# Kernel optimization log

Hardware: AMD Instinct MI355X
Metric: run time of the kernel (lower is better)

Reference implementation:

```python
import jax, jax.numpy as jnp
import numpy as np

MAX_DIST = 32  # unidirectional T5-style bucketing: num_buckets = 33
N_HEAD, D_K, D_V = 8, 64, 64


def setup_inputs() -> dict:
    key = jax.random.key(0)
    ks = jax.random.split(key, 9)
    B, S, D = 4, 2048, 512
    q = jax.random.normal(ks[0], (B, S, D), dtype=jnp.float32)
    k = jax.random.normal(ks[1], (B, S, D), dtype=jnp.float32)
    v = jax.random.normal(ks[2], (B, S, D), dtype=jnp.float32)
    mask = jax.random.randint(ks[3], (B, 1, 1, S), 0, 2, dtype=jnp.int32)
    sc = 1.0 / np.sqrt(D)
    Wq = jax.random.normal(ks[4], (D, D), dtype=jnp.float32) * sc
    Wk = jax.random.normal(ks[5], (D, D), dtype=jnp.float32) * sc
    Wv = jax.random.normal(ks[6], (D, D), dtype=jnp.float32) * sc
    Wfc = jax.random.normal(ks[7], (D, D), dtype=jnp.float32) * sc
    rel_bias = jax.random.normal(ks[8], (MAX_DIST + 1, N_HEAD), dtype=jnp.float32)
    return {"q": q, "k": k, "v": v, "mask": mask, "Wq": Wq, "Wk": Wk,
            "Wv": Wv, "Wfc": Wfc, "rel_bias": rel_bias}


def _rel_pos_bias(rel_bias, seq_len):
    # unidirectional: bucket = clamp(max(context - memory, 0), 0, MAX_DIST)
    pos = jnp.arange(seq_len)
    n = pos[:, None] - pos[None, :]              # context - memory = -relative_position
    bucket = jnp.clip(jnp.maximum(n, 0), 0, MAX_DIST)
    vals = rel_bias[bucket]                      # (S, S, H)
    return jnp.transpose(vals, (2, 0, 1))[None]  # (1, H, S, S)


def reference(q, k, v, mask, Wq, Wk, Wv, Wfc, rel_bias):
    B, Sq, _ = q.shape
    Sk = k.shape[1]
    scale = D_K ** (-0.5)
    qh = (q @ Wq).reshape(B, Sq, N_HEAD, D_K).transpose(0, 2, 1, 3)  # bhsd
    kh = (k @ Wk).reshape(B, Sk, N_HEAD, D_K).transpose(0, 2, 1, 3)
    vh = (v @ Wv).reshape(B, Sk, N_HEAD, D_V).transpose(0, 2, 1, 3)
    attn = jnp.einsum('bhqd,bhkd->bhqk', qh, kh) * scale
    attn = attn + _rel_pos_bias(rel_bias, Sq)
    attn = jnp.where(mask == 0, jnp.float32(-1e9), attn)
    attn = jax.nn.softmax(attn, axis=-1)          # dropout is identity at eval
    out = jnp.einsum('bhqk,bhkd->bhqd', attn, vh)
    out = out.transpose(0, 2, 1, 3).reshape(B, Sq, N_HEAD * D_V)
    out = out @ Wfc
    return out, attn
```

## Files before the change

kernel.cpp:

```cpp
#include <hip/hip_runtime.h>
#include <hip/hip_bf16.h>


typedef __attribute__((ext_vector_type(8))) short bfrag;
typedef __attribute__((ext_vector_type(4))) float f32x4;
typedef unsigned int u32;

#define MFMA16(a,b,c) __builtin_amdgcn_mfma_f32_16x16x32_bf16(a,b,c,0,0,0)

#define BAR() do{ asm volatile("s_waitcnt lgkmcnt(0)" ::: "memory"); \
                  __builtin_amdgcn_s_barrier(); }while(0)

__device__ __forceinline__ void gl_lds16(const void* g, void* l){
  __builtin_amdgcn_global_load_lds((const __attribute__((address_space(1))) u32*)g,
                                   (__attribute__((address_space(3))) u32*)l, 16, 0, 0);
}
__device__ __forceinline__ short f2bs(float f){
  u32 u = __float_as_uint(f);
  u = (u + 0x7fffu + ((u>>16)&1u)) >> 16;
  return (short)u;
}
__device__ __forceinline__ float b2f(short s){
  return __uint_as_float(((u32)(unsigned short)s) << 16);
}
__device__ __forceinline__ u32 pack2(float a, float b){
  float2 t; t.x = a; t.y = b;
  __hip_bfloat162 h = __float22bfloat162_rn(t);
  return *(u32*)&h;
}

#define BB 4
#define HH 8
#define SS 2048
#define DD 512

#define WQT_OFF  0u
#define WKT_OFF  524288u
#define WVT_OFF  1048576u
#define WFCT_OFF 1572864u
#define QB_OFF   2097152u
#define KB_OFF   10485760u
#define VB_OFF   18874368u
#define QH_OFF   27262976u
#define KH_OFF   35651584u
#define VT_OFF   44040192u
#define OH_OFF   52428800u

__global__ __launch_bounds__(256) void conv_w_k(const float* w0,const float* w1,
                                                const float* w2,const float* w3, char* ws){
  const float* w; short* o;
  switch(blockIdx.z){
    case 0:  w=w0; o=(short*)(ws+WQT_OFF); break;
    case 1:  w=w1; o=(short*)(ws+WKT_OFF); break;
    case 2:  w=w2; o=(short*)(ws+WVT_OFF); break;
    default: w=w3; o=(short*)(ws+WFCT_OFF); break;
  }
  int t  = blockIdx.x*256 + threadIdx.x;
  int n  = t >> 6;
  int k0 = (t & 63) << 3;
  bfrag v;
  #pragma unroll
  for (int j=0;j<8;++j) v[j] = f2bs(w[(k0+j)*512 + n]);
  *(bfrag*)(o + n*512 + k0) = v;
}

__global__ __launch_bounds__(256) void conv_x_k(const float* x0,const float* x1,
                                                const float* x2, char* ws){
  const float* x; short* o;
  switch(blockIdx.z){
    case 0:  x=x0; o=(short*)(ws+QB_OFF); break;
    case 1:  x=x1; o=(short*)(ws+KB_OFF); break;
    default: x=x2; o=(short*)(ws+VB_OFF); break;
  }
  int i = (blockIdx.x*256 + threadIdx.x) << 3;
  float4 a = *(const float4*)(x+i);
  float4 b = *(const float4*)(x+i+4);
  bfrag v;
  v[0]=f2bs(a.x); v[1]=f2bs(a.y); v[2]=f2bs(a.z); v[3]=f2bs(a.w);
  v[4]=f2bs(b.x); v[5]=f2bs(b.y); v[6]=f2bs(b.z); v[7]=f2bs(b.w);
  *(bfrag*)(o+i) = v;
}

__device__ void gemm_core(const short* A, const short* Bt, char* Cout, int mode, int bid){
  __shared__ __align__(16) char lds[32768];
  int i0, j0;
  if (mode==1){ i0 = (bid&3)<<7; j0 = (bid>>2)<<7; }
  else        { i0 = (bid>>2)<<7; j0 = (bid&3)<<7; }
  int tid = threadIdx.x;
  int l = tid & 63, w = tid >> 6;
  int wr = (w>>1)<<6, wc = (w&1)<<6;
  int l15 = l & 15, l4 = l >> 4;
  f32x4 acc[4][4];
  #pragma unroll
  for(int a=0;a<4;++a)
    #pragma unroll
    for(int b=0;b<4;++b) acc[a][b] = (f32x4){0.f,0.f,0.f,0.f};
  const char* Ab = (const char*)A;
  const char* Bb = (const char*)Bt;
  for (int kk=0; kk<8; ++kk){
    #pragma unroll
    for (int it=0; it<4; ++it){
      int ci = it*256 + tid;
      int row = ci>>3, cc = ci&7;
      gl_lds16(Ab + (size_t)(i0+row)*1024 + kk*128 + ((cc^(row&7))<<4),
               lds + ((it*256 + w*64)<<4));
      gl_lds16(Bb + (size_t)(j0+row)*1024 + kk*128 + ((cc^(row&7))<<4),
               lds + 16384 + ((it*256 + w*64)<<4));
    }
    asm volatile("s_waitcnt vmcnt(0)" ::: "memory");
    __syncthreads();
    #pragma unroll
    for (int kb=0; kb<2; ++kb){
      bfrag af[4], bf[4];
      #pragma unroll
      for (int mi=0;mi<4;++mi){
        int row = wr + mi*16 + l15;
        af[mi] = *(const bfrag*)(lds + row*128 + (((kb*4 + l4) ^ (row&7))<<4));
      }
      #pragma unroll
      for (int ni=0;ni<4;++ni){
        int row = wc + ni*16 + l15;
        bf[ni] = *(const bfrag*)(lds + 16384 + row*128 + (((kb*4 + l4) ^ (row&7))<<4));
      }
      #pragma unroll
      for (int mi=0;mi<4;++mi)
        #pragma unroll
        for (int ni=0;ni<4;++ni)
          acc[mi][ni] = MFMA16(af[mi], bf[ni], acc[mi][ni]);
    }
    __syncthreads();
  }
  #pragma unroll
  for (int mi=0;mi<4;++mi){
    #pragma unroll
    for (int ni=0;ni<4;++ni){
      #pragma unroll
      for (int r=0;r<4;++r){
        int i = i0 + wr + mi*16 + (l4<<2) + r;
        int j = j0 + wc + ni*16 + l15;
        float v = acc[mi][ni][r];
        if (mode==2){
          ((float*)Cout)[(size_t)i*512 + j] = v;
        } else if (mode==0){
          size_t o = ((size_t)(((i>>11)<<3) + (j>>6))*2048 + (size_t)(i&2047))*64 + (j&63);
          ((short*)Cout)[o] = f2bs(v);
        } else {
          size_t o = ((size_t)(((j>>11)<<3) + (i>>6))*64 + (size_t)(i&63))*2048 + (j&2047);
          ((short*)Cout)[o] = f2bs(v);
        }
      }
    }
  }
}

__global__ __launch_bounds__(256,2) void gemm_proj_k(char* ws){
  switch(blockIdx.z){
    case 0:  gemm_core((const short*)(ws+QB_OFF),  (const short*)(ws+WQT_OFF), ws+QH_OFF, 0, blockIdx.x); break;
    case 1:  gemm_core((const short*)(ws+KB_OFF),  (const short*)(ws+WKT_OFF), ws+KH_OFF, 0, blockIdx.x); break;
    default: gemm_core((const short*)(ws+WVT_OFF), (const short*)(ws+VB_OFF),  ws+VT_OFF, 1, blockIdx.x); break;
  }
}
__global__ __launch_bounds__(256,2) void gemm_final_k(char* ws, float* out){
  gemm_core((const short*)(ws+OH_OFF), (const short*)(ws+WFCT_OFF), (char*)out, 2, blockIdx.x);
}

#define MSK_OFF_L   65536
#define BIAS_OFF_L  73728
#define WSUM_OFF_L  73872
#define RECIP_OFF_L 74384
#define LDS_TOTAL   74496

__global__ __launch_bounds__(512,4) void attn_k(char* ws, const int* mask,
                                                const float* rel_bias, float* attn_out){
  extern __shared__ __align__(16) char sm[];
  int tid = threadIdx.x;
  int l = tid & 63, w = tid >> 6;
  int l15 = l & 15, l4 = l >> 4;
  int bh = blockIdx.x, qblk = blockIdx.y;
  int b = bh >> 3, h = bh & 7;
  const short* qhb = (const short*)(ws+QH_OFF) + (size_t)bh*SS*64;
  const char*  khb = ws + KH_OFF + (size_t)bh*SS*128;
  const char*  vtb = ws + VT_OFF + (size_t)bh*64*SS*2;

  {
    const int4* m4 = (const int4*)(mask + b*SS);
    int4 ma = m4[tid];
    float4* mf = (float4*)(sm + MSK_OFF_L);
    mf[tid] = make_float4(ma.x?1.f:0.f, ma.y?1.f:0.f, ma.z?1.f:0.f, ma.w?1.f:0.f);
  }
  if (tid < 33) ((float*)(sm+BIAS_OFF_L))[tid] = rel_bias[tid*HH + h];
  float bias0  = rel_bias[h];
  float bias32 = rel_bias[32*HH + h];
  const float* biasl = (const float*)(sm+BIAS_OFF_L);
  const float* maskl = (const float*)(sm+MSK_OFF_L);

  int qrow = (qblk<<4) + l15;
  bfrag qA0 = *(const bfrag*)(qhb + (size_t)qrow*64 + l4*8);
  bfrag qA1 = *(const bfrag*)(qhb + (size_t)qrow*64 + 32 + l4*8);
  int r0 = qblk<<4;
  int wbase = w << 8;

  __syncthreads();

  float rs = 0.f;
  #pragma unroll 2
  for (int t=0; t<16; ++t){
    int c0 = wbase + (t<<4);
    const char* kr = khb + (size_t)(c0 + l15)*128 + (l4<<4);
    bfrag b0 = *(const bfrag*)(kr);
    bfrag b1 = *(const bfrag*)(kr + 64);
    f32x4 acc = (f32x4){0.f,0.f,0.f,0.f};
    acc = MFMA16(b0, qA0, acc);
    acc = MFMA16(b1, qA1, acc);
    float4 m4v = *(const float4*)(maskl + c0 + (l4<<2));
    float pr[4];
    if (c0 >= r0+16){
      #pragma unroll
      for (int r=0;r<4;++r) pr[r] = __expf(acc[r]*0.125f + bias0);
    } else if (c0 <= r0-47){
      #pragma unroll
      for (int r=0;r<4;++r) pr[r] = __expf(acc[r]*0.125f + bias32);
    } else {
      #pragma unroll
      for (int r=0;r<4;++r){
        int n = (r0 + l15) - (c0 + (l4<<2) + r);
        n = n<0 ? 0 : (n>32 ? 32 : n);
        pr[r] = __expf(acc[r]*0.125f + biasl[n]);
      }
    }
    float p0 = m4v.x*pr[0], p1 = m4v.y*pr[1], p2 = m4v.z*pr[2], p3 = m4v.w*pr[3];
    rs += (p0+p1)+(p2+p3);
    int byte = (c0 + (l4<<2)) << 1;
    int ch = (byte>>4) ^ l15;
    uint2 pk; pk.x = pack2(p0,p1); pk.y = pack2(p2,p3);
    *(uint2*)(sm + l15*4096 + (ch<<4) + (byte&15)) = pk;
  }

  {
    rs += __shfl_xor(rs, 16);
    rs += __shfl_xor(rs, 32);
    float* wsum = (float*)(sm+WSUM_OFF_L);
    if (l < 16) wsum[(w<<4) + l15] = rs;
  }
  BAR();
  if (tid < 16){
    float* wsum = (float*)(sm+WSUM_OFF_L);
    float t2 = 0.f;
    #pragma unroll
    for (int i=0;i<8;++i) t2 += wsum[(i<<4) + tid];
    ((float*)(sm+RECIP_OFF_L))[tid] = 1.f/t2;
  }
  BAR();
  const float* recip = (const float*)(sm+RECIP_OFF_L);

  if (w < 4){
    f32x4 acco = (f32x4){0.f,0.f,0.f,0.f};
    int dbase = w<<4;
    const char* vr = vtb + (size_t)(dbase + l15)*4096 + (l4<<4);
    #pragma unroll 4
    for (int kt=0; kt<64; ++kt){
      int ch = ((kt<<2) + l4) ^ l15;
      bfrag af = *(const bfrag*)(sm + l15*4096 + (ch<<4));
      bfrag bv = *(const bfrag*)(vr + (kt<<6));
      acco = MFMA16(af, bv, acco);
    }
    short* oh = (short*)(ws + OH_OFF);
    #pragma unroll
    for (int r=0;r<4;++r){
      int rowl = (l4<<2) + r;
      float rc = recip[rowl];
      size_t sg = (size_t)b*SS + (qblk<<4) + rowl;
      oh[sg*512 + h*64 + dbase + l15] = f2bs(acco[r]*rc);
    }
  } else {
    int sw = w - 4;
    float* attb = attn_out + (size_t)bh*SS*SS + (size_t)(r0)*SS;
    #pragma unroll 4
    for (int i=0; i<32; ++i){
      int row = (sw<<2) + (i&3);
      int c   = i>>2;
      float rc = recip[row];
      int byte = (c<<9) + (l<<3);
      int ch = (byte>>4) ^ row;
      uint2 pk = *(const uint2*)(sm + row*4096 + (ch<<4) + (byte&15));
      short s0 = (short)(pk.x & 0xffff), s1 = (short)(pk.x >> 16);
      short s2 = (short)(pk.y & 0xffff), s3 = (short)(pk.y >> 16);
      f32x4 o = (f32x4){ b2f(s0)*rc, b2f(s1)*rc, b2f(s2)*rc, b2f(s3)*rc };
      *(f32x4*)(attb + (size_t)row*SS + (c<<8) + (l<<2)) = o;
    }
  }
}

extern "C" void kernel_launch(void* const* d_in, const int* in_sizes, int n_in,
                              void* d_out, int out_size, void* d_ws, size_t ws_size,
                              hipStream_t stream){
  const float* q   = (const float*)d_in[0];
  const float* k   = (const float*)d_in[1];
  const float* v   = (const float*)d_in[2];
  const int*  mask = (const int*)  d_in[3];
  const float* Wq  = (const float*)d_in[4];
  const float* Wk  = (const float*)d_in[5];
  const float* Wv  = (const float*)d_in[6];
  const float* Wfc = (const float*)d_in[7];
  const float* rb  = (const float*)d_in[8];
  char* ws = (char*)d_ws;
  float* out  = (float*)d_out;
  float* attn = out + (size_t)BB*SS*512;

  (void)hipFuncSetAttribute((const void*)attn_k,
        hipFuncAttributeMaxDynamicSharedMemorySize, LDS_TOTAL);

  conv_w_k<<<dim3(128,1,4), 256, 0, stream>>>(Wq, Wk, Wv, Wfc, ws);
  conv_x_k<<<dim3(2048,1,3), 256, 0, stream>>>(q, k, v, ws);
  gemm_proj_k<<<dim3(256,1,3), 256, 0, stream>>>(ws);
  attn_k<<<dim3(32,128), 512, LDS_TOTAL, stream>>>(ws, mask, rb, attn);
  gemm_final_k<<<dim3(256,1,1), 256, 0, stream>>>(ws, out);
}
```

Measured before the change: 349.8 us.

## Split attention-prob writeout into bf16 workspace stage and separate streaming expand kernel

The attention kernel now writes unnormalized bf16 probabilities and per-row reciprocals to workspace with nontemporal stores, rather than expanding to fp32 and writing the large attn output itself. A new streaming kernel then reads the bf16 buffer, applies the reciprocal and writes fp32 attn. The aim is to decouple the bandwidth-heavy fp32 store from the compute kernel's occupancy. The cost is an extra 268 MB round trip of bf16 data through workspace plus one more launch.

```diff
diff --git a/kernel.cpp b/kernel.cpp
--- a/kernel.cpp
+++ b/kernel.cpp
@@ -5,6 +5,7 @@
 typedef __attribute__((ext_vector_type(8))) short bfrag;
 typedef __attribute__((ext_vector_type(4))) float f32x4;
 typedef unsigned int u32;
+typedef __attribute__((ext_vector_type(4))) u32 u32x4;
 
 #define MFMA16(a,b,c) __builtin_amdgcn_mfma_f32_16x16x32_bf16(a,b,c,0,0,0)
 
@@ -45,6 +46,8 @@
 #define KH_OFF   35651584u
 #define VT_OFF   44040192u
 #define OH_OFF   52428800u
+#define PW_OFF   67108864u
+#define RECIPW_OFF 335544320u
 
 __global__ __launch_bounds__(256) void conv_w_k(const float* w0,const float* w1,
                                                 const float* w2,const float* w3, char* ws){
@@ -170,8 +173,8 @@
 #define RECIP_OFF_L 74384
 #define LDS_TOTAL   74496
 
-__global__ __launch_bounds__(512,4) void attn_k(char* ws, const int* mask,
-                                                const float* rel_bias, float* attn_out){
+__global__ __launch_bounds__(512,4) void attn_compute_k(char* ws, const int* mask,
+                                                        const float* rel_bias){
   extern __shared__ __align__(16) char sm[];
   int tid = threadIdx.x;
   int l = tid & 63, w = tid >> 6;
@@ -248,7 +251,9 @@
     float t2 = 0.f;
     #pragma unroll
     for (int i=0;i<8;++i) t2 += wsum[(i<<4) + tid];
-    ((float*)(sm+RECIP_OFF_L))[tid] = 1.f/t2;
+    float rv = 1.f/t2;
+    ((float*)(sm+RECIP_OFF_L))[tid] = rv;
+    ((float*)(ws+RECIPW_OFF))[(bh<<11) + r0 + tid] = rv;
   }
   BAR();
   const float* recip = (const float*)(sm+RECIP_OFF_L);
@@ -274,20 +279,32 @@
     }
   } else {
     int sw = w - 4;
-    float* attb = attn_out + (size_t)bh*SS*SS + (size_t)(r0)*SS;
+    char* pdst = ws + PW_OFF + ((size_t)bh*SS + r0)*SS*2;
     #pragma unroll 4
-    for (int i=0; i<32; ++i){
+    for (int i=0; i<16; ++i){
       int row = (sw<<2) + (i&3);
       int c   = i>>2;
-      float rc = recip[row];
-      int byte = (c<<9) + (l<<3);
+      int byte = (c<<10) + (l<<4);
       int ch = (byte>>4) ^ row;
-      uint2 pk = *(const uint2*)(sm + row*4096 + (ch<<4) + (byte&15));
-      short s0 = (short)(pk.x & 0xffff), s1 = (short)(pk.x >> 16);
-      short s2 = (short)(pk.y & 0xffff), s3 = (short)(pk.y >> 16);
-      f32x4 o = (f32x4){ b2f(s0)*rc, b2f(s1)*rc, b2f(s2)*rc, b2f(s3)*rc };
-      *(f32x4*)(attb + (size_t)row*SS + (c<<8) + (l<<2)) = o;
-    }
+      u32x4 pk = *(const u32x4*)(sm + row*4096 + (ch<<4));
+      __builtin_nontemporal_store(pk, (u32x4*)(pdst + (size_t)row*4096 + byte));
+    }
+  }
+}
+
+__global__ __launch_bounds__(256) void attn_stream_k(const char* wsc, float* attn){
+  const ushort* p = (const ushort*)(wsc + PW_OFF);
+  const float* recip = (const float*)(wsc + RECIPW_OFF);
+  size_t idx = (((size_t)blockIdx.x<<8) + threadIdx.x) << 2;
+  const size_t stride = (size_t)4096*256*4;
+  #pragma unroll 4
+  for (int it=0; it<32; ++it, idx += stride){
+    uint2 pk = *(const uint2*)(p + idx);
+    float rc = recip[idx>>11];
+    short s0 = (short)(pk.x & 0xffff), s1 = (short)(pk.x >> 16);
+    short s2 = (short)(pk.y & 0xffff), s3 = (short)(pk.y >> 16);
+    f32x4 o = (f32x4){ b2f(s0)*rc, b2f(s1)*rc, b2f(s2)*rc, b2f(s3)*rc };
+    *(f32x4*)(attn + idx) = o;
   }
 }
 
@@ -307,12 +324,13 @@
   float* out  = (float*)d_out;
   float* attn = out + (size_t)BB*SS*512;
 
-  (void)hipFuncSetAttribute((const void*)attn_k,
+  (void)hipFuncSetAttribute((const void*)attn_compute_k,
         hipFuncAttributeMaxDynamicSharedMemorySize, LDS_TOTAL);
 
   conv_w_k<<<dim3(128,1,4), 256, 0, stream>>>(Wq, Wk, Wv, Wfc, ws);
   conv_x_k<<<dim3(2048,1,3), 256, 0, stream>>>(q, k, v, ws);
   gemm_proj_k<<<dim3(256,1,3), 256, 0, stream>>>(ws);
-  attn_k<<<dim3(32,128), 512, LDS_TOTAL, stream>>>(ws, mask, rb, attn);
+  attn_compute_k<<<dim3(32,128), 512, LDS_TOTAL, stream>>>(ws, mask, rb);
+  attn_stream_k<<<dim3(4096), 256, 0, stream>>>(ws, attn);
   gemm_final_k<<<dim3(256,1,1), 256, 0, stream>>>(ws, out);
 }
```

New measurement: 479.2 us. 37.0% more time.
